# Kernel tuning notes

Measured on AMD Instinct MI355X. Metric: run time of the kernel, lower is better.

The kernel has to match this reference:

```python
import jax, jax.numpy as jnp
import numpy as np

D_MODEL = 1024
NUM_HEADS = 16
MAX_LEN = 512  # chunk_size
BATCH = 2
SEQ_LEN = 2048


def _mha(x, w_in, b_in, w_out, b_out, num_heads):
    """torch.nn.MultiheadAttention (eval mode, self-attn) over the last-but-one axis.
    x: (..., S, d). Packed in-proj weight w_in: (3d, d), out-proj w_out: (d, d)."""
    *batch, S, d = x.shape
    hd = d // num_heads
    qkv = x @ w_in.T + b_in                      # (..., S, 3d)
    q, k, v = jnp.split(qkv, 3, axis=-1)
    def heads(t):
        return t.reshape(*batch, S, num_heads, hd)
    q, k, v = heads(q), heads(k), heads(v)
    scale = 1.0 / np.sqrt(hd).astype(np.float32)
    scores = jnp.einsum('...qhd,...khd->...hqk', q, k) * scale
    attn = jax.nn.softmax(scores, axis=-1)
    o = jnp.einsum('...hqk,...khd->...qhd', attn, v).reshape(*batch, S, d)
    return o @ w_out.T + b_out


def setup_inputs() -> dict:
    key = jax.random.key(0)
    ks = jax.random.split(key, 5)
    d = D_MODEL
    s = 0.02
    return {
        'x': jax.random.normal(ks[0], (BATCH, SEQ_LEN, d), dtype=jnp.float32),
        'w_in_l': jax.random.normal(ks[1], (3 * d, d), dtype=jnp.float32) * s,
        'b_in_l': jnp.zeros((3 * d,), jnp.float32),
        'w_out_l': jax.random.normal(ks[2], (d, d), dtype=jnp.float32) * s,
        'b_out_l': jnp.zeros((d,), jnp.float32),
        'w_in_g': jax.random.normal(ks[3], (3 * d, d), dtype=jnp.float32) * s,
        'b_in_g': jnp.zeros((3 * d,), jnp.float32),
        'w_out_g': jax.random.normal(ks[4], (d, d), dtype=jnp.float32) * s,
        'b_out_g': jnp.zeros((d,), jnp.float32),
    }


def reference(x, w_in_l, b_in_l, w_out_l, b_out_l, w_in_g, b_in_g, w_out_g, b_out_g):
    B, S, d = x.shape
    cs = MAX_LEN
    nc = S // cs
    # (B, nc, cs, d) -> (B, cs, nc, d): for each intra-chunk position, attend across chunks.
    xc = x.reshape(B, nc, cs, d).transpose(0, 2, 1, 3)
    # Vectorized replacement for the python loop over chunk positions:
    # batched MHA with batch (B, cs) and sequence length nc.
    loc = _mha(xc, w_in_l, b_in_l, w_out_l, b_out_l, NUM_HEADS)  # (B, cs, nc, d)
    # Faithful to torch: stack -> (nc, cs, B, d), transpose(1,2) -> (nc, B, cs, d),
    # then raw reshape to (B, S, d) (a layout-reinterpreting view, preserved here).
    loc = loc.transpose(2, 0, 1, 3).reshape(B, S, d)
    # Global full self-attention over the whole sequence.
    return _mha(loc, w_in_g, b_in_g, w_out_g, b_out_g, NUM_HEADS)
```

## Files before the change

kernel.cpp:

```cpp
#include <hip/hip_runtime.h>

#define BB 2
#define SS 2048
#define DD 1024
#define HH 16
#define HD 64
#define CS 512
#define NC 4
#define TD 3072
#define MM 4096

typedef __attribute__((ext_vector_type(8))) short short8;
typedef __attribute__((ext_vector_type(4))) float floatx4;

__device__ __forceinline__ float bf2f(unsigned short h) {
  union { unsigned int u; float f; } v; v.u = ((unsigned int)h) << 16; return v.f;
}
__device__ __forceinline__ unsigned short f2bf(float f) {
  union { float f; unsigned int u; } v; v.f = f;
  unsigned int r = (v.u + 0x7fffu + ((v.u >> 16) & 1u)) >> 16;
  return (unsigned short)r;
}
__device__ __forceinline__ short8 ld8f(const float* p) {
  floatx4 f0 = *(const floatx4*)p;
  floatx4 f1 = *(const floatx4*)(p + 4);
  short8 o;
  o[0] = (short)f2bf(f0[0]); o[1] = (short)f2bf(f0[1]);
  o[2] = (short)f2bf(f0[2]); o[3] = (short)f2bf(f0[3]);
  o[4] = (short)f2bf(f1[0]); o[5] = (short)f2bf(f1[1]);
  o[6] = (short)f2bf(f1[2]); o[7] = (short)f2bf(f1[3]);
  return o;
}
__device__ __forceinline__ short8 scale8_eighth(short8 a) {
  short8 o;
#pragma unroll
  for (int j = 0; j < 8; ++j) o[j] = (short)f2bf(bf2f((unsigned short)a[j]) * 0.125f);
  return o;
}
__device__ __forceinline__ void async16(const void* g, void* l) {
  __builtin_amdgcn_global_load_lds((const __attribute__((address_space(1))) void*)g,
                                   (__attribute__((address_space(3))) void*)l, 16, 0, 0);
}

__global__ __launch_bounds__(256) void cvt_all(
    const float* __restrict__ s0, unsigned short* __restrict__ d0, int n0,
    const float* __restrict__ s1, unsigned short* __restrict__ d1, int n1,
    const float* __restrict__ s2, unsigned short* __restrict__ d2, int n2,
    const float* __restrict__ s3, unsigned short* __restrict__ d3, int n3) {
  int bb = blockIdx.x;
  const float* s; unsigned short* d; int off;
  if (bb < n0) { s = s0; d = d0; off = bb; }
  else if (bb < n0 + n1) { s = s1; d = d1; off = bb - n0; }
  else if (bb < n0 + n1 + n2) { s = s2; d = d2; off = bb - n0 - n1; }
  else { s = s3; d = d3; off = bb - n0 - n1 - n2; }
  int i = (off * 256 + threadIdx.x) * 8;
  *(short8*)(d + i) = ld8f(s + i);
}

__global__ __launch_bounds__(256) void cvt_bf16(const float* __restrict__ in,
                                                unsigned short* __restrict__ out, int n) {
  int i = (blockIdx.x * 256 + threadIdx.x) * 8;
  if (i < n) *(short8*)(out + i) = ld8f(in + i);
}

template <int MT, int C_F32>
__global__ __launch_bounds__(256) void gemm_bt_bias(
    const unsigned short* __restrict__ A, const unsigned short* __restrict__ W,
    const float* __restrict__ bias, void* __restrict__ Cv, int M, int N, int K) {
  constexpr int AI = MT / 32;
  __shared__ unsigned short sA[MT * 32];
  __shared__ unsigned short sB[128 * 32];
  const int tid = threadIdx.x;
  const int wid = tid >> 6, lane = tid & 63;
  const int quad = lane >> 4, l15 = lane & 15;
  const int wm = wid & 1, wn = wid >> 1;
  const int bm = blockIdx.y, bn = blockIdx.x;

  floatx4 acc[AI][4];
#pragma unroll
  for (int i = 0; i < AI; ++i)
#pragma unroll
    for (int j = 0; j < 4; ++j) acc[i][j] = (floatx4){0.f, 0.f, 0.f, 0.f};

  const int r = tid >> 2;
  const int kc = (tid & 3) * 8;
  const unsigned short* gA = A + (size_t)(bm * MT + r) * K + kc;
  const unsigned short* gW = W + (size_t)(bn * 128 + r) * K + kc;
  unsigned short* lA = sA + wid * 512;
  unsigned short* lB = sB + wid * 512;

  for (int k0 = 0; k0 < K; k0 += 32) {
#pragma unroll
    for (int s = 0; s < MT / 64; ++s)
      async16(gA + (size_t)(s * 64) * K + k0, lA + s * 2048);
    async16(gW + k0, lB);
    async16(gW + (size_t)64 * K + k0, lB + 2048);
    __syncthreads();

    short8 af[AI], bfr[4];
#pragma unroll
    for (int i = 0; i < AI; ++i)
      af[i] = *(const short8*)(sA + (wm * (MT / 2) + i * 16 + l15) * 32 + quad * 8);
#pragma unroll
    for (int j = 0; j < 4; ++j)
      bfr[j] = *(const short8*)(sB + (wn * 64 + j * 16 + l15) * 32 + quad * 8);
#pragma unroll
    for (int i = 0; i < AI; ++i)
#pragma unroll
      for (int j = 0; j < 4; ++j)
        acc[i][j] = __builtin_amdgcn_mfma_f32_16x16x32_bf16(af[i], bfr[j], acc[i][j], 0, 0, 0);
    __syncthreads();
  }

#pragma unroll
  for (int j = 0; j < 4; ++j) {
    int n = bn * 128 + wn * 64 + j * 16 + l15;
    float bv = bias[n];
#pragma unroll
    for (int i = 0; i < AI; ++i) {
      int mrow = bm * MT + wm * (MT / 2) + i * 16 + quad * 4;
#pragma unroll
      for (int rr = 0; rr < 4; ++rr) {
        float v = acc[i][j][rr] + bv;
        if (C_F32) ((float*)Cv)[(size_t)(mrow + rr) * N + n] = v;
        else ((unsigned short*)Cv)[(size_t)(mrow + rr) * N + n] = f2bf(v);
      }
    }
  }
}

__global__ __launch_bounds__(256) void attn_local(const unsigned short* __restrict__ QKV,
                                                  unsigned short* __restrict__ O) {
  const int tid = threadIdx.x;
  const int wid = tid >> 6, lane = tid & 63;
  const int idx = blockIdx.x * 4 + wid;
  const int h = idx & 15, c = (idx >> 4) & 511, b = idx >> 13;

  float q[NC], k[NC], v[NC];
#pragma unroll
  for (int n = 0; n < NC; ++n) {
    size_t base = (size_t)(b * SS + n * CS + c) * TD + h * HD + lane;
    q[n] = bf2f(QKV[base]);
    k[n] = bf2f(QKV[base + DD]);
    v[n] = bf2f(QKV[base + 2 * DD]);
  }
  float s[NC][NC];
#pragma unroll
  for (int m = 0; m < NC; ++m)
#pragma unroll
    for (int n = 0; n < NC; ++n) {
      float p = q[m] * k[n];
#pragma unroll
      for (int off = 32; off >= 1; off >>= 1) p += __shfl_xor(p, off);
      s[m][n] = p * 0.125f;
    }
#pragma unroll
  for (int m = 0; m < NC; ++m) {
    float mx = fmaxf(fmaxf(s[m][0], s[m][1]), fmaxf(s[m][2], s[m][3]));
    float e[NC], sum = 0.f;
#pragma unroll
    for (int n = 0; n < NC; ++n) { e[n] = __expf(s[m][n] - mx); sum += e[n]; }
    float o = (e[0] * v[0] + e[1] * v[1] + e[2] * v[2] + e[3] * v[3]) / sum;
    O[(size_t)(m * (BB * CS) + b * CS + c) * DD + h * HD + lane] = f2bf(o);
  }
}

__global__ __launch_bounds__(256) void transpose_v(const unsigned short* __restrict__ QKV,
                                                   unsigned short* __restrict__ VT) {
  __shared__ unsigned short sT[64 * 64];
  const int tid = threadIdx.x;
  const int bh = blockIdx.x, b = bh >> 4, h = bh & 15;
  const int s0 = blockIdx.y * 64;
#pragma unroll
  for (int it = 0; it < 2; ++it) {
    int C = it * 256 + tid;
    int t = C >> 3, dc = C & 7;
    short8 v = *(const short8*)(QKV + (size_t)(b * SS + s0 + t) * TD + 2 * DD + h * HD + dc * 8);
    *(short8*)(sT + t * 64 + ((dc ^ (t & 7)) << 3)) = v;
  }
  __syncthreads();
#pragma unroll
  for (int it = 0; it < 2; ++it) {
    int C = it * 256 + tid;
    int d = C >> 3, tc = C & 7;
    short8 o;
#pragma unroll
    for (int j = 0; j < 8; ++j) {
      int t = tc * 8 + j;
      o[j] = (short)sT[t * 64 + (((d >> 3) ^ (t & 7)) << 3) + (d & 7)];
    }
    *(short8*)(VT + ((size_t)(bh * 64 + d)) * SS + s0 + tc * 8) = o;
  }
}

__global__ __launch_bounds__(256, 3) void attn_global(
    const unsigned short* __restrict__ Q, const unsigned short* __restrict__ Kp,
    const unsigned short* __restrict__ VT, unsigned short* __restrict__ O) {
  __shared__ unsigned short sK[2][64 * 64];
  __shared__ unsigned short sVT[2][64 * 64];
  __shared__ unsigned short sP[4][32 * 64];
  __shared__ float lsumBuf[64];
  const int tid = threadIdx.x;
  const int wid = tid >> 6, lane = tid & 63;
  const int quad = lane >> 4, l15 = lane & 15;
  const int qhalf = wid & 1, khalf = wid >> 1;
  const int bh = blockIdx.x;
  const int b = bh >> 4, h = bh & 15;
  const int q0 = blockIdx.y * 64 + qhalf * 32;

  short8 qf[2][2];
#pragma unroll
  for (int g = 0; g < 2; ++g) {
    const unsigned short* qr = Q + (size_t)(b * SS + q0 + g * 16 + l15) * TD + h * HD + quad * 8;
    qf[g][0] = scale8_eighth(*(const short8*)qr);
    qf[g][1] = scale8_eighth(*(const short8*)(qr + 32));
  }

  float lsum[2][4];
  floatx4 oacc[2][4];
#pragma unroll
  for (int g = 0; g < 2; ++g)
#pragma unroll
    for (int s = 0; s < 4; ++s) { lsum[g][s] = 0.f; oacc[g][s] = (floatx4){0.f, 0.f, 0.f, 0.f}; }

  unsigned short* myP = &sP[wid][0];
  const unsigned short* myK = &sK[khalf][0];
  const unsigned short* myV = &sVT[khalf][0];
  const unsigned short* vbase = VT + (size_t)(bh * 64) * SS;

  const unsigned short* gK[4]; unsigned short* lK[4];
  const unsigned short* gV[4]; unsigned short* lV[4];
#pragma unroll
  for (int kh = 0; kh < 2; ++kh)
#pragma unroll
    for (int it = 0; it < 2; ++it) {
      const int j = kh * 2 + it;
      const int P = it * 256 + tid;
      const int row = P >> 3, c8 = P & 7;
      gK[j] = Kp + (size_t)(b * SS + kh * 1024 + row) * TD + h * HD + c8 * 8;
      lK[j] = &sK[kh][0] + row * 64 + ((c8 ^ (row & 7)) << 3);
      gV[j] = vbase + (size_t)row * SS + kh * 1024 + c8 * 8;
      lV[j] = &sVT[kh][0] + row * 64 + ((c8 ^ (row & 7)) << 3);
    }

  short8 rK[4], rV[4];
#pragma unroll
  for (int j = 0; j < 4; ++j) { rK[j] = *(const short8*)gK[j]; rV[j] = *(const short8*)gV[j]; }
#pragma unroll
  for (int j = 0; j < 4; ++j) { *(short8*)lK[j] = rK[j]; *(short8*)lV[j] = rV[j]; }
  __syncthreads();

  for (int t = 0; t < 16; ++t) {
    if (t < 15) {
#pragma unroll
      for (int j = 0; j < 4; ++j) {
        rK[j] = *(const short8*)(gK[j] + (size_t)(t + 1) * (64 * TD));
        rV[j] = *(const short8*)(gV[j] + (t + 1) * 64);
      }
    }
    __builtin_amdgcn_sched_barrier(0);

    floatx4 sacc[2][4];
    __builtin_amdgcn_s_setprio(1);
#pragma unroll
    for (int sub = 0; sub < 4; ++sub) {
      int key = sub * 16 + l15;
      int c0 = (quad ^ (key & 7)) << 3;
      short8 kf0 = *(const short8*)(myK + key * 64 + c0);
      short8 kf1 = *(const short8*)(myK + key * 64 + (c0 ^ 32));
#pragma unroll
      for (int g = 0; g < 2; ++g) {
        floatx4 z = (floatx4){0.f, 0.f, 0.f, 0.f};
        z = __builtin_amdgcn_mfma_f32_16x16x32_bf16(qf[g][0], kf0, z, 0, 0, 0);
        z = __builtin_amdgcn_mfma_f32_16x16x32_bf16(qf[g][1], kf1, z, 0, 0, 0);
        sacc[g][sub] = z;
      }
    }
    __builtin_amdgcn_s_setprio(0);

#pragma unroll
    for (int g = 0; g < 2; ++g)
#pragma unroll
      for (int sub = 0; sub < 4; ++sub) {
        int kc8 = sub * 2 + (l15 >> 3), k7 = l15 & 7;
#pragma unroll
        for (int rr = 0; rr < 4; ++rr) {
          unsigned int u = __float_as_uint(__expf(sacc[g][sub][rr]));
          lsum[g][rr] += __uint_as_float(u & 0xffff0000u);
          int row = g * 16 + quad * 4 + rr;
          myP[row * 64 + ((kc8 ^ (row & 7)) << 3) + k7] = (unsigned short)(u >> 16);
        }
      }
    __asm__ volatile("s_waitcnt lgkmcnt(0)" ::: "memory");

    short8 pf[2][2];
#pragma unroll
    for (int g = 0; g < 2; ++g) {
      int row = g * 16 + l15;
      int sw = row & 7;
#pragma unroll
      for (int c = 0; c < 2; ++c)
        pf[g][c] = *(const short8*)(myP + row * 64 + (((c * 4 + quad) ^ sw) << 3));
    }

    __builtin_amdgcn_s_setprio(1);
#pragma unroll
    for (int sub = 0; sub < 4; ++sub) {
      int n = sub * 16 + l15;
      int v0 = (quad ^ (n & 7)) << 3;
      short8 vt0 = *(const short8*)(myV + n * 64 + v0);
      short8 vt1 = *(const short8*)(myV + n * 64 + (v0 ^ 32));
#pragma unroll
      for (int g = 0; g < 2; ++g) {
        oacc[g][sub] = __builtin_amdgcn_mfma_f32_16x16x32_bf16(pf[g][0], vt0, oacc[g][sub], 0, 0, 0);
        oacc[g][sub] = __builtin_amdgcn_mfma_f32_16x16x32_bf16(pf[g][1], vt1, oacc[g][sub], 0, 0, 0);
      }
    }
    __builtin_amdgcn_s_setprio(0);
    __syncthreads();

    if (t < 15) {
#pragma unroll
      for (int j = 0; j < 4; ++j) { *(short8*)lK[j] = rK[j]; *(short8*)lV[j] = rV[j]; }
    }
    __syncthreads();
  }

  float lred[2][4];
#pragma unroll
  for (int g = 0; g < 2; ++g)
#pragma unroll
    for (int rr = 0; rr < 4; ++rr) {
      float t = lsum[g][rr];
#pragma unroll
      for (int off = 8; off >= 1; off >>= 1) t += __shfl_xor(t, off);
      lred[g][rr] = t;
    }

  float* obuf = (float*)&sP[0][0];
  if (khalf == 1) {
    float* my = obuf + qhalf * 2048;
#pragma unroll
    for (int g = 0; g < 2; ++g)
#pragma unroll
      for (int sub = 0; sub < 4; ++sub)
#pragma unroll
        for (int rr = 0; rr < 4; ++rr)
          my[(g * 16 + quad * 4 + rr) * 64 + sub * 16 + l15] = oacc[g][sub][rr];
    if (l15 == 0)
#pragma unroll
      for (int g = 0; g < 2; ++g)
#pragma unroll
        for (int rr = 0; rr < 4; ++rr)
          lsumBuf[qhalf * 32 + g * 16 + quad * 4 + rr] = lred[g][rr];
  }
  __syncthreads();
  if (khalf == 0) {
    float* my = obuf + qhalf * 2048;
#pragma unroll
    for (int g = 0; g < 2; ++g) {
#pragma unroll
      for (int rr = 0; rr < 4; ++rr)
        lred[g][rr] = 1.f / (lred[g][rr] + lsumBuf[qhalf * 32 + g * 16 + quad * 4 + rr]);
#pragma unroll
      for (int sub = 0; sub < 4; ++sub)
#pragma unroll
        for (int rr = 0; rr < 4; ++rr) {
          float v = oacc[g][sub][rr] + my[(g * 16 + quad * 4 + rr) * 64 + sub * 16 + l15];
          int row = b * SS + q0 + g * 16 + quad * 4 + rr;
          O[(size_t)row * DD + h * HD + sub * 16 + l15] = f2bf(v * lred[g][rr]);
        }
    }
  }
}

extern "C" void kernel_launch(void* const* d_in, const int* in_sizes, int n_in,
                              void* d_out, int out_size, void* d_ws, size_t ws_size,
                              hipStream_t stream) {
  const float* x       = (const float*)d_in[0];
  const float* w_in_l  = (const float*)d_in[1];
  const float* b_in_l  = (const float*)d_in[2];
  const float* w_out_l = (const float*)d_in[3];
  const float* b_out_l = (const float*)d_in[4];
  const float* w_in_g  = (const float*)d_in[5];
  const float* b_in_g  = (const float*)d_in[6];
  const float* w_out_g = (const float*)d_in[7];
  const float* b_out_g = (const float*)d_in[8];

  unsigned short* wsA = (unsigned short*)d_ws;
  unsigned short* wsB = wsA + (size_t)MM * TD;
  unsigned short* dob = (unsigned short*)d_out;
  unsigned short* wbf_out_l = dob;
  unsigned short* wbf_in_g  = dob + (size_t)DD * DD;
  unsigned short* wbf_in_l  = dob + 4 * (size_t)DD * DD;
  unsigned short* o1        = dob + 4 * (size_t)DD * DD;
  unsigned short* vtbuf     = dob;

  dim3 blk(256);
  cvt_all<<<dim3(5632), blk, 0, stream>>>(w_out_l, wbf_out_l, 512,
                                          w_in_g, wbf_in_g, 1536,
                                          w_in_l, wbf_in_l, 1536,
                                          x, wsB, 2048);

  gemm_bt_bias<128, 0><<<dim3(TD / 128, MM / 128), blk, 0, stream>>>(wsB, wbf_in_l, b_in_l, wsA, MM, TD, DD);
  attn_local<<<dim3(BB * CS * HH / 4), blk, 0, stream>>>(wsA, o1);
  gemm_bt_bias<64, 0><<<dim3(DD / 128, MM / 64), blk, 0, stream>>>(o1, wbf_out_l, b_out_l, wsB, MM, DD, DD);
  gemm_bt_bias<128, 0><<<dim3(TD / 128, MM / 128), blk, 0, stream>>>(wsB, wbf_in_g, b_in_g, wsA, MM, TD, DD);
  transpose_v<<<dim3(BB * HH, SS / 64), blk, 0, stream>>>(wsA, vtbuf);
  attn_global<<<dim3(BB * HH, SS / 64), blk, 0, stream>>>(wsA, wsA + DD, vtbuf, wsB);
  cvt_bf16<<<dim3(DD * DD / 2048), blk, 0, stream>>>(w_out_g, wsA, DD * DD);
  gemm_bt_bias<64, 1><<<dim3(DD / 128, MM / 64), blk, 0, stream>>>(wsB, wsA, b_out_g, d_out, MM, DD, DD);
}
```

Measured before the change: 360.0 us.

## Double-buffer K via async global-to-LDS loads and read V directly from global

```diff
diff --git a/kernel.cpp b/kernel.cpp
--- a/kernel.cpp
+++ b/kernel.cpp
@@ -193,11 +193,10 @@
   }
 }
 
-__global__ __launch_bounds__(256, 3) void attn_global(
+__global__ __launch_bounds__(256) void attn_global(
     const unsigned short* __restrict__ Q, const unsigned short* __restrict__ Kp,
     const unsigned short* __restrict__ VT, unsigned short* __restrict__ O) {
-  __shared__ unsigned short sK[2][64 * 64];
-  __shared__ unsigned short sVT[2][64 * 64];
+  __shared__ unsigned short sK[2][2][64 * 64];
   __shared__ unsigned short sP[4][32 * 64];
   __shared__ float lsumBuf[64];
   const int tid = threadIdx.x;
@@ -224,41 +223,38 @@
     for (int s = 0; s < 4; ++s) { lsum[g][s] = 0.f; oacc[g][s] = (floatx4){0.f, 0.f, 0.f, 0.f}; }
 
   unsigned short* myP = &sP[wid][0];
-  const unsigned short* myK = &sK[khalf][0];
-  const unsigned short* myV = &sVT[khalf][0];
-  const unsigned short* vbase = VT + (size_t)(bh * 64) * SS;
-
-  const unsigned short* gK[4]; unsigned short* lK[4];
-  const unsigned short* gV[4]; unsigned short* lV[4];
+
+  const unsigned short* srcK[4];
+  unsigned short* dstK[4];
 #pragma unroll
   for (int kh = 0; kh < 2; ++kh)
 #pragma unroll
     for (int it = 0; it < 2; ++it) {
       const int j = kh * 2 + it;
       const int P = it * 256 + tid;
-      const int row = P >> 3, c8 = P & 7;
-      gK[j] = Kp + (size_t)(b * SS + kh * 1024 + row) * TD + h * HD + c8 * 8;
-      lK[j] = &sK[kh][0] + row * 64 + ((c8 ^ (row & 7)) << 3);
-      gV[j] = vbase + (size_t)row * SS + kh * 1024 + c8 * 8;
-      lV[j] = &sVT[kh][0] + row * 64 + ((c8 ^ (row & 7)) << 3);
-    }
-
-  short8 rK[4], rV[4];
-#pragma unroll
-  for (int j = 0; j < 4; ++j) { rK[j] = *(const short8*)gK[j]; rV[j] = *(const short8*)gV[j]; }
-#pragma unroll
-  for (int j = 0; j < 4; ++j) { *(short8*)lK[j] = rK[j]; *(short8*)lV[j] = rV[j]; }
+      const int key = P >> 3, dcg = (P & 7) ^ (key & 7);
+      srcK[j] = Kp + (size_t)(b * SS + kh * 1024 + key) * TD + h * HD + dcg * 8;
+      dstK[j] = &sK[0][kh][0] + it * 2048 + wid * 512;
+    }
+  const size_t kstride = (size_t)64 * TD;
+
+  const unsigned short* vrow[4];
+#pragma unroll
+  for (int sub = 0; sub < 4; ++sub)
+    vrow[sub] = VT + (size_t)(bh * 64 + sub * 16 + l15) * SS + khalf * 1024 + quad * 8;
+
+#pragma unroll
+  for (int j = 0; j < 4; ++j) { async16(srcK[j], dstK[j]); srcK[j] += kstride; }
   __syncthreads();
 
   for (int t = 0; t < 16; ++t) {
+    const int cur = t & 1;
     if (t < 15) {
-#pragma unroll
-      for (int j = 0; j < 4; ++j) {
-        rK[j] = *(const short8*)(gK[j] + (size_t)(t + 1) * (64 * TD));
-        rV[j] = *(const short8*)(gV[j] + (t + 1) * 64);
-      }
-    }
-    __builtin_amdgcn_sched_barrier(0);
+      const int nb = ((t + 1) & 1) * 8192;
+#pragma unroll
+      for (int j = 0; j < 4; ++j) { async16(srcK[j], dstK[j] + nb); srcK[j] += kstride; }
+    }
+    const unsigned short* myK = &sK[cur][khalf][0];
 
     floatx4 sacc[2][4];
     __builtin_amdgcn_s_setprio(1);
@@ -277,6 +273,14 @@
       }
     }
     __builtin_amdgcn_s_setprio(0);
+
+    short8 vt0[4], vt1[4];
+#pragma unroll
+    for (int sub = 0; sub < 4; ++sub) {
+      vt0[sub] = *(const short8*)(vrow[sub]);
+      vt1[sub] = *(const short8*)(vrow[sub] + 32);
+      vrow[sub] += 64;
+    }
 
 #pragma unroll
     for (int g = 0; g < 2; ++g)
@@ -306,23 +310,13 @@
     __builtin_amdgcn_s_setprio(1);
 #pragma unroll
     for (int sub = 0; sub < 4; ++sub) {
-      int n = sub * 16 + l15;
-      int v0 = (quad ^ (n & 7)) << 3;
-      short8 vt0 = *(const short8*)(myV + n * 64 + v0);
-      short8 vt1 = *(const short8*)(myV + n * 64 + (v0 ^ 32));
 #pragma unroll
       for (int g = 0; g < 2; ++g) {
-        oacc[g][sub] = __builtin_amdgcn_mfma_f32_16x16x32_bf16(pf[g][0], vt0, oacc[g][sub], 0, 0, 0);
-        oacc[g][sub] = __builtin_amdgcn_mfma_f32_16x16x32_bf16(pf[g][1], vt1, oacc[g][sub], 0, 0, 0);
+        oacc[g][sub] = __builtin_amdgcn_mfma_f32_16x16x32_bf16(pf[g][0], vt0[sub], oacc[g][sub], 0, 0, 0);
+        oacc[g][sub] = __builtin_amdgcn_mfma_f32_16x16x32_bf16(pf[g][1], vt1[sub], oacc[g][sub], 0, 0, 0);
       }
     }
     __builtin_amdgcn_s_setprio(0);
-    __syncthreads();
-
-    if (t < 15) {
-#pragma unroll
-      for (int j = 0; j < 4; ++j) { *(short8*)lK[j] = rK[j]; *(short8*)lV[j] = rV[j]; }
-    }
     __syncthreads();
   }
 
```

After: 364.6 us. About the same (+1.3%).
